# Performance work log

Hardware: AMD Instinct MI355X
Metric: run time of the kernel (lower is better)

The kernel has to match this reference:

```python
import jax, jax.numpy as jnp
import numpy as np

N_NODES = 100000


def _graph_conv(x, W, b, src, dst, n_nodes):
    # DGL GraphConv, norm='both':
    #   h = x * out_deg(src)^{-1/2}; h = h @ W; agg = scatter_sum over dst;
    #   out = agg * in_deg(dst)^{-1/2} + b
    ones = jnp.ones(src.shape, dtype=x.dtype)
    out_deg = jax.ops.segment_sum(ones, src, num_segments=n_nodes)
    in_deg = jax.ops.segment_sum(ones, dst, num_segments=n_nodes)
    norm_src = jax.lax.rsqrt(jnp.maximum(out_deg, 1.0))  # [N]
    norm_dst = jax.lax.rsqrt(jnp.maximum(in_deg, 1.0))   # [N]
    h = (x * norm_src[:, None]) @ W                      # [N, hid]
    msgs = h[src]                                        # [E, hid] gather
    agg = jax.ops.segment_sum(msgs, dst, num_segments=n_nodes)  # [N, hid]
    return jax.nn.relu(agg * norm_dst[:, None] + b)


def setup_inputs() -> dict:
    key = jax.random.key(0)
    k1, k2, k3, k4, k5 = jax.random.split(key, 5)
    n, e, d = N_NODES, 1600000, 128
    x = jax.random.normal(k1, (n, d), dtype=jnp.float32)
    src = jax.random.randint(k2, (e,), 0, n, dtype=jnp.int32)
    dst = jax.random.randint(k3, (e,), 0, n, dtype=jnp.int32)
    # Xavier-ish init for GraphConv weights, zero bias (DGL default)
    W1 = jax.random.normal(k4, (d, d), dtype=jnp.float32) / np.sqrt(d)
    W2 = jax.random.normal(k5, (d, d), dtype=jnp.float32) / np.sqrt(d)
    b1 = jnp.zeros((d,), dtype=jnp.float32)
    b2 = jnp.zeros((d,), dtype=jnp.float32)
    return {"x": x, "W1": W1, "b1": b1, "W2": W2, "b2": b2, "src": src, "dst": dst}


def reference(x, W1, b1, W2, b2, src, dst):
    h = _graph_conv(x, W1, b1, src, dst, N_NODES)
    h = _graph_conv(h, W2, b2, src, dst, N_NODES)
    return h
```

## Files before the change

### kernel.cpp

```cpp
#include <hip/hip_runtime.h>
#include <hip/hip_fp16.h>

#define HD 128
#define CHUNK 4096
#define MAXNB 512

__global__ __launch_bounds__(256) void count_src4(const int* __restrict__ src,
                                                  unsigned int* __restrict__ cnt4s,
                                                  int N, int E) {
    int t = blockIdx.x * 256 + threadIdx.x;
    int e0 = t * 4;
    if (e0 >= E) return;
    if (e0 + 3 < E) {
        int4 s4 = ((const int4*)src)[t];
        atomicAdd(&cnt4s[0 * N + s4.x], 1u);
        atomicAdd(&cnt4s[1 * N + s4.y], 1u);
        atomicAdd(&cnt4s[2 * N + s4.z], 1u);
        atomicAdd(&cnt4s[3 * N + s4.w], 1u);
    } else {
        for (int j = 0; e0 + j < E; ++j)
            atomicAdd(&cnt4s[j * N + src[e0 + j]], 1u);
    }
}

__global__ __launch_bounds__(256) void make_norm_src(const unsigned int* __restrict__ cnt4s,
                                                     float* __restrict__ norm_src, int N) {
    int i = blockIdx.x * 256 + threadIdx.x;
    if (i < N) {
        float od = (float)(cnt4s[i] + cnt4s[N + i] + cnt4s[2 * N + i] + cnt4s[3 * N + i]);
        norm_src[i] = rsqrtf(od > 1.f ? od : 1.f);
    }
}

__global__ __launch_bounds__(256) void hist_coarse(const int* __restrict__ dst,
                                                   unsigned int* __restrict__ gHist,
                                                   int NB, int NC, int E) {
    __shared__ unsigned int hist[MAXNB];
    for (int b = threadIdx.x; b < NB; b += 256) hist[b] = 0;
    __syncthreads();
    int chunk = blockIdx.x;
    int base = chunk * CHUNK;
    int end = base + CHUNK < E ? base + CHUNK : E;
    for (int e = base + threadIdx.x; e < end; e += 256)
        atomicAdd(&hist[dst[e] >> 8], 1u);
    __syncthreads();
    for (int b = threadIdx.x; b < NB; b += 256)
        gHist[(size_t)b * NC + chunk] = hist[b];
}

__global__ __launch_bounds__(256) void scan_a(const unsigned int* __restrict__ cnt,
                                              unsigned int* __restrict__ excl,
                                              unsigned int* __restrict__ bsum, int n) {
    int i = blockIdx.x * 256 + threadIdx.x;
    unsigned int v = (i < n) ? cnt[i] : 0u;
    unsigned int x = v;
#pragma unroll
    for (int d = 1; d < 64; d <<= 1) {
        unsigned int y = __shfl_up(x, d, 64);
        if ((threadIdx.x & 63) >= d) x += y;
    }
    __shared__ unsigned int wsum[4];
    if ((threadIdx.x & 63) == 63) wsum[threadIdx.x >> 6] = x;
    __syncthreads();
    unsigned int woff = 0;
    for (int w = 0; w < (int)(threadIdx.x >> 6); ++w) woff += wsum[w];
    unsigned int incl = x + woff;
    if (i < n) excl[i] = incl - v;
    if (threadIdx.x == 255) bsum[blockIdx.x] = incl;
}

__global__ __launch_bounds__(1024) void scan_b(const unsigned int* __restrict__ bsum,
                                               unsigned int* __restrict__ boff, int nb) {
    int t = threadIdx.x;
    unsigned int v = (t < nb) ? bsum[t] : 0u;
    unsigned int x = v;
#pragma unroll
    for (int d = 1; d < 64; d <<= 1) {
        unsigned int y = __shfl_up(x, d, 64);
        if ((t & 63) >= d) x += y;
    }
    __shared__ unsigned int wsum[16];
    if ((t & 63) == 63) wsum[t >> 6] = x;
    __syncthreads();
    unsigned int woff = 0;
    for (int w = 0; w < (t >> 6); ++w) woff += wsum[w];
    unsigned int incl = x + woff;
    if (t < nb) boff[t] = incl - v;
}

__global__ __launch_bounds__(256) void scan_c(unsigned int* __restrict__ excl,
                                              const unsigned int* __restrict__ boff, int n) {
    int i = blockIdx.x * 256 + threadIdx.x;
    if (i < n) excl[i] += boff[blockIdx.x];
}

__global__ __launch_bounds__(256) void scatter_coarse(const int* __restrict__ src,
                                                      const int* __restrict__ dst,
                                                      const unsigned int* __restrict__ scanA,
                                                      unsigned int* __restrict__ packed,
                                                      int NB, int NC, int E) {
    __shared__ unsigned int curs[MAXNB];
    int chunk = blockIdx.x;
    for (int b = threadIdx.x; b < NB; b += 256)
        curs[b] = scanA[(size_t)b * NC + chunk];
    __syncthreads();
    int base = chunk * CHUNK;
    int end = base + CHUNK < E ? base + CHUNK : E;
    for (int e = base + threadIdx.x; e < end; e += 256) {
        int d = dst[e];
        int s = src[e];
        unsigned int pos = atomicAdd(&curs[d >> 8], 1u);
        packed[pos] = ((unsigned int)(d & 255) << 24) | (unsigned int)s;
    }
}

__global__ __launch_bounds__(256) void fine_sort(const unsigned int* __restrict__ packed,
                                                 const unsigned int* __restrict__ scanA,
                                                 int* __restrict__ sorted_src,
                                                 unsigned int* __restrict__ offsets,
                                                 unsigned int* __restrict__ cntg,
                                                 float* __restrict__ normd,
                                                 int NB, int NC, int N, int E) {
    __shared__ unsigned int cnt[256];
    __shared__ unsigned int curs[256];
    __shared__ unsigned int wsum[4];
    int b = blockIdx.x;
    int t = threadIdx.x;
    unsigned int S = scanA[(size_t)b * NC];
    unsigned int T = (b + 1 < NB) ? scanA[(size_t)(b + 1) * NC] : (unsigned int)E;
    cnt[t] = 0;
    __syncthreads();
    for (unsigned int j = S + t; j < T; j += 256)
        atomicAdd(&cnt[packed[j] >> 24], 1u);
    __syncthreads();
    unsigned int v = cnt[t], x = v;
    int lane = t & 63;
#pragma unroll
    for (int d = 1; d < 64; d <<= 1) {
        unsigned int y = __shfl_up(x, d, 64);
        if (lane >= d) x += y;
    }
    if (lane == 63) wsum[t >> 6] = x;
    __syncthreads();
    unsigned int woff = 0;
    for (int w = 0; w < (t >> 6); ++w) woff += wsum[w];
    unsigned int ex = x - v + woff;
    curs[t] = ex;
    int node = b * 256 + t;
    if (node < N) {
        offsets[node] = S + ex;
        cntg[node] = v;
        float f = (float)v;
        normd[node] = rsqrtf(f > 1.f ? f : 1.f);
    }
    __syncthreads();
    for (unsigned int j = S + t; j < T; j += 256) {
        unsigned int p = packed[j];
        unsigned int pos = S + atomicAdd(&curs[p >> 24], 1u);
        sorted_src[pos] = (int)(p & 0xFFFFFFu);
    }
}

__global__ __launch_bounds__(256) void prep_x(const float* __restrict__ x,
                                              const float* __restrict__ norm,
                                              __half* __restrict__ xh, int total) {
    int t = blockIdx.x * 256 + threadIdx.x;
    if (t >= total) return;
    int row = t >> 5;
    float nr = norm[row];
    float4 v = ((const float4*)x)[t];
    __half2 lo = __floats2half2_rn(v.x * nr, v.y * nr);
    __half2 hi = __floats2half2_rn(v.z * nr, v.w * nr);
    uint2 pk;
    pk.x = *(unsigned int*)&lo;
    pk.y = *(unsigned int*)&hi;
    ((uint2*)xh)[t] = pk;
}

__global__ __launch_bounds__(256) void gemm_h(const __half* __restrict__ xh,
                                              const float* __restrict__ W,
                                              __half* __restrict__ h, int n) {
    __shared__ __half2 Wh[HD * 64];
    __shared__ float  xs[64][HD];
    const int tid = threadIdx.x;

    {
        const float4* W4 = (const float4*)W;
#pragma unroll
        for (int i = 0; i < 16; ++i) {
            int idx = tid + 256 * i;
            float4 wv = W4[idx];
            __half2 a = __floats2half2_rn(wv.x, wv.y);
            __half2 b = __floats2half2_rn(wv.z, wv.w);
            int k = idx >> 5, c4 = idx & 31;
            Wh[k * 64 + c4 * 2]     = a;
            Wh[k * 64 + c4 * 2 + 1] = b;
        }
    }
    const int row0 = blockIdx.x * 64;
    {
#pragma unroll
        for (int i = 0; i < 8; ++i) {
            int idx = i * 256 + tid;
            int r = idx >> 5, c = idx & 31;
            int row = row0 + r;
            uint2 u = make_uint2(0u, 0u);
            if (row < n) u = ((const uint2*)xh)[(size_t)row * 32 + c];
            float2 f0 = __half22float2(*(const __half2*)&u.x);
            float2 f1 = __half22float2(*(const __half2*)&u.y);
            ((float4*)xs[r])[c] = make_float4(f0.x, f0.y, f1.x, f1.y);
        }
    }
    __syncthreads();

    const int g  = tid >> 5;
    const int c4 = tid & 31;

    float4 acc[8];
#pragma unroll
    for (int j = 0; j < 8; ++j) acc[j] = make_float4(0.f, 0.f, 0.f, 0.f);

    for (int k = 0; k < HD; k += 2) {
        uint2 w0 = *(const uint2*)&Wh[k * 64 + c4 * 2];
        uint2 w1 = *(const uint2*)&Wh[(k + 1) * 64 + c4 * 2];
        float2 wa0 = __half22float2(*(const __half2*)&w0.x);
        float2 wb0 = __half22float2(*(const __half2*)&w0.y);
        float2 wa1 = __half22float2(*(const __half2*)&w1.x);
        float2 wb1 = __half22float2(*(const __half2*)&w1.y);
#pragma unroll
        for (int j = 0; j < 8; ++j) {
            float2 xk = *(const float2*)&xs[g * 8 + j][k];
            acc[j].x = fmaf(xk.x, wa0.x, acc[j].x);
            acc[j].y = fmaf(xk.x, wa0.y, acc[j].y);
            acc[j].z = fmaf(xk.x, wb0.x, acc[j].z);
            acc[j].w = fmaf(xk.x, wb0.y, acc[j].w);
            acc[j].x = fmaf(xk.y, wa1.x, acc[j].x);
            acc[j].y = fmaf(xk.y, wa1.y, acc[j].y);
            acc[j].z = fmaf(xk.y, wb1.x, acc[j].z);
            acc[j].w = fmaf(xk.y, wb1.y, acc[j].w);
        }
    }

#pragma unroll
    for (int j = 0; j < 8; ++j) {
        int row = row0 + g * 8 + j;
        if (row < n) {
            __half2 lo = __floats2half2_rn(acc[j].x, acc[j].y);
            __half2 hi = __floats2half2_rn(acc[j].z, acc[j].w);
            uint2 pk;
            pk.x = *(unsigned int*)&lo;
            pk.y = *(unsigned int*)&hi;
            ((uint2*)(h + (size_t)row * HD))[c4] = pk;
        }
    }
}

template <bool MID>
__global__ __launch_bounds__(256) void aggregate_k(const __half* __restrict__ h,
                                                   const int* __restrict__ sorted_src,
                                                   const unsigned int* __restrict__ offsets,
                                                   const unsigned int* __restrict__ cnt,
                                                   const float* __restrict__ norm_dst,
                                                   const float* __restrict__ nsrc,
                                                   const float* __restrict__ bias,
                                                   float* __restrict__ outF,
                                                   __half* __restrict__ outH, int n) {
    int node = blockIdx.x * 4 + (int)(threadIdx.x >> 6);
    if (node >= n) return;
    int lane = threadIdx.x & 63;
    int g   = lane >> 4;
    int sub = lane & 15;

    unsigned int start = offsets[node];
    unsigned int deg   = cnt[node];
    const int* sp = sorted_src + start;
    const uint4* h4 = (const uint4*)h;

    float acc[8];
#pragma unroll
    for (int j = 0; j < 8; ++j) acc[j] = 0.f;

#define ACCUM(u)                                                                  \
    { float2 f;                                                                   \
      f = __half22float2(*(const __half2*)&(u).x); acc[0] += f.x; acc[1] += f.y;  \
      f = __half22float2(*(const __half2*)&(u).y); acc[2] += f.x; acc[3] += f.y;  \
      f = __half22float2(*(const __half2*)&(u).z); acc[4] += f.x; acc[5] += f.y;  \
      f = __half22float2(*(const __half2*)&(u).w); acc[6] += f.x; acc[7] += f.y; }

    unsigned int i = 0;
    for (; i + 16 <= deg; i += 16) {
        int s0 = sp[i + g];
        int s1 = sp[i + 4 + g];
        int s2 = sp[i + 8 + g];
        int s3 = sp[i + 12 + g];
        uint4 u0 = h4[(size_t)s0 * 16 + sub];
        uint4 u1 = h4[(size_t)s1 * 16 + sub];
        uint4 u2 = h4[(size_t)s2 * 16 + sub];
        uint4 u3 = h4[(size_t)s3 * 16 + sub];
        ACCUM(u0);
        ACCUM(u1);
        ACCUM(u2);
        ACCUM(u3);
    }
    for (; i < deg; i += 4) {
        if (i + g < deg) {
            int s = sp[i + g];
            uint4 u = h4[(size_t)s * 16 + sub];
            ACCUM(u);
        }
    }
#undef ACCUM

#pragma unroll
    for (int j = 0; j < 8; ++j) {
        acc[j] += __shfl_xor(acc[j], 16, 64);
        acc[j] += __shfl_xor(acc[j], 32, 64);
    }

    float nd = norm_dst[node];
    int col2 = sub * 4 + g;
    float2 bb = ((const float2*)bias)[col2];
    float vx = fmaxf(fmaf(acc[g * 2 + 0], nd, bb.x), 0.f);
    float vy = fmaxf(fmaf(acc[g * 2 + 1], nd, bb.y), 0.f);
    if (MID) {
        float ns = nsrc[node];
        __half2 p = __floats2half2_rn(vx * ns, vy * ns);
        ((__half2*)outH)[(size_t)node * 64 + col2] = p;
    } else {
        ((float2*)outF)[(size_t)node * 64 + col2] = make_float2(vx, vy);
    }
}

extern "C" void kernel_launch(void* const* d_in, const int* in_sizes, int n_in,
                              void* d_out, int out_size, void* d_ws, size_t ws_size,
                              hipStream_t stream) {
    const float* x   = (const float*)d_in[0];
    const float* W1  = (const float*)d_in[1];
    const float* b1  = (const float*)d_in[2];
    const float* W2  = (const float*)d_in[3];
    const float* b2  = (const float*)d_in[4];
    const int*   src = (const int*)d_in[5];
    const int*   dst = (const int*)d_in[6];

    const int N = in_sizes[0] / HD;
    const int E = in_sizes[5];
    float* out = (float*)d_out;

    const int NB = (N + 255) / 256;
    const int NC = (E + CHUNK - 1) / CHUNK;
    const int scanLen = NB * NC;
    const int nbS = (scanLen + 255) / 256;
    const int nbN = (N + 255) / 256;

    float*        norm_src = (float*)d_ws;
    float*        normd    = norm_src + N;
    unsigned int* cntg     = (unsigned int*)(normd + N);
    unsigned int* offsets  = cntg + N;
    unsigned int* cnt4s    = offsets + N;
    unsigned int* gHist    = cnt4s + 4 * N;
    unsigned int* scanA    = gHist + scanLen;
    unsigned int* bsum     = scanA + scanLen;
    unsigned int* boff     = bsum + 1024;
    unsigned int* packed   = boff + 1024;
    int*          sorted   = (int*)(packed + E);
    __half*       h        = (__half*)(sorted + E);
    __half*       xh       = h + (size_t)N * HD;

    hipMemsetAsync(cnt4s, 0, (size_t)4 * N * 4, stream);
    count_src4<<<(E / 4 + 255) / 256, 256, 0, stream>>>(src, cnt4s, N, E);
    make_norm_src<<<nbN, 256, 0, stream>>>(cnt4s, norm_src, N);
    hist_coarse<<<NC, 256, 0, stream>>>(dst, gHist, NB, NC, E);
    scan_a<<<nbS, 256, 0, stream>>>(gHist, scanA, bsum, scanLen);
    scan_b<<<1, 1024, 0, stream>>>(bsum, boff, nbS);
    scan_c<<<nbS, 256, 0, stream>>>(scanA, boff, scanLen);
    scatter_coarse<<<NC, 256, 0, stream>>>(src, dst, scanA, packed, NB, NC, E);
    fine_sort<<<NB, 256, 0, stream>>>(packed, scanA, sorted, offsets, cntg, normd, NB, NC, N, E);

    prep_x<<<(N * 32 + 255) / 256, 256, 0, stream>>>(x, norm_src, xh, N * 32);
    gemm_h<<<(N + 63) / 64, 256, 0, stream>>>(xh, W1, h, N);
    aggregate_k<true><<<(N + 3) / 4, 256, 0, stream>>>(h, sorted, offsets, cntg, normd,
                                                       norm_src, b1, nullptr, xh, N);

    gemm_h<<<(N + 63) / 64, 256, 0, stream>>>(xh, W2, h, N);
    aggregate_k<false><<<(N + 3) / 4, 256, 0, stream>>>(h, sorted, offsets, cntg, normd,
                                                        nullptr, b2, out, nullptr, N);
}
```

Measured before the change: 398.3 us.

## Use MFMA fp16 GEMM with pre-transposed weights and fuse degree histograms

Replaces the scalar-FMA LDS-tiled GEMM with a register-only MFMA 16x16x32 f16 kernel. It reads x rows and pre-transposed fp16 weights, which a new prep_w kernel builds once for both layers. The src out-degree count and the coarse dst histogram now run in one kernel, so there is one fewer launch and the edge arrays are read in a single pass. Buffers are padded to a multiple of 64 rows so the GEMM can read rows past N without bounds checks. The risk is that weight fragments now come from global/L2 memory and are not shared in LDS.

```diff
diff --git a/kernel.cpp b/kernel.cpp
--- a/kernel.cpp
+++ b/kernel.cpp
@@ -5,22 +5,43 @@
 #define CHUNK 4096
 #define MAXNB 512
 
-__global__ __launch_bounds__(256) void count_src4(const int* __restrict__ src,
+typedef _Float16 f16x8 __attribute__((ext_vector_type(8)));
+typedef float f32x4 __attribute__((ext_vector_type(4)));
+
+__global__ __launch_bounds__(256) void hist_count(const int* __restrict__ src,
+                                                  const int* __restrict__ dst,
                                                   unsigned int* __restrict__ cnt4s,
-                                                  int N, int E) {
-    int t = blockIdx.x * 256 + threadIdx.x;
-    int e0 = t * 4;
-    if (e0 >= E) return;
-    if (e0 + 3 < E) {
-        int4 s4 = ((const int4*)src)[t];
-        atomicAdd(&cnt4s[0 * N + s4.x], 1u);
-        atomicAdd(&cnt4s[1 * N + s4.y], 1u);
-        atomicAdd(&cnt4s[2 * N + s4.z], 1u);
-        atomicAdd(&cnt4s[3 * N + s4.w], 1u);
-    } else {
-        for (int j = 0; e0 + j < E; ++j)
-            atomicAdd(&cnt4s[j * N + src[e0 + j]], 1u);
-    }
+                                                  unsigned int* __restrict__ gHist,
+                                                  int N, int NB, int NC, int E) {
+    __shared__ unsigned int hist[MAXNB];
+    for (int b = threadIdx.x; b < NB; b += 256) hist[b] = 0;
+    __syncthreads();
+    int base = blockIdx.x * CHUNK;
+    int e0 = base + 4 * threadIdx.x;
+#pragma unroll
+    for (int it = 0; it < CHUNK / 1024; ++it, e0 += 1024) {
+        if (e0 + 3 < E) {
+            int4 s4 = *(const int4*)(src + e0);
+            int4 d4 = *(const int4*)(dst + e0);
+            atomicAdd(&cnt4s[0 * N + s4.x], 1u);
+            atomicAdd(&cnt4s[1 * N + s4.y], 1u);
+            atomicAdd(&cnt4s[2 * N + s4.z], 1u);
+            atomicAdd(&cnt4s[3 * N + s4.w], 1u);
+            atomicAdd(&hist[d4.x >> 8], 1u);
+            atomicAdd(&hist[d4.y >> 8], 1u);
+            atomicAdd(&hist[d4.z >> 8], 1u);
+            atomicAdd(&hist[d4.w >> 8], 1u);
+        } else {
+            for (int j = 0; j < 4; ++j)
+                if (e0 + j < E) {
+                    atomicAdd(&cnt4s[j * N + src[e0 + j]], 1u);
+                    atomicAdd(&hist[dst[e0 + j] >> 8], 1u);
+                }
+        }
+    }
+    __syncthreads();
+    for (int b = threadIdx.x; b < NB; b += 256)
+        gHist[(size_t)b * NC + blockIdx.x] = hist[b];
 }
 
 __global__ __launch_bounds__(256) void make_norm_src(const unsigned int* __restrict__ cnt4s,
@@ -32,20 +53,15 @@
     }
 }
 
-__global__ __launch_bounds__(256) void hist_coarse(const int* __restrict__ dst,
-                                                   unsigned int* __restrict__ gHist,
-                                                   int NB, int NC, int E) {
-    __shared__ unsigned int hist[MAXNB];
-    for (int b = threadIdx.x; b < NB; b += 256) hist[b] = 0;
-    __syncthreads();
-    int chunk = blockIdx.x;
-    int base = chunk * CHUNK;
-    int end = base + CHUNK < E ? base + CHUNK : E;
-    for (int e = base + threadIdx.x; e < end; e += 256)
-        atomicAdd(&hist[dst[e] >> 8], 1u);
-    __syncthreads();
-    for (int b = threadIdx.x; b < NB; b += 256)
-        gHist[(size_t)b * NC + chunk] = hist[b];
+__global__ __launch_bounds__(256) void prep_w(const float* __restrict__ W1,
+                                              const float* __restrict__ W2,
+                                              _Float16* __restrict__ Wt) {
+    const float* W = blockIdx.x ? W2 : W1;
+    _Float16* T = Wt + (size_t)blockIdx.x * HD * HD;
+    for (int i = threadIdx.x; i < HD * HD; i += 256) {
+        int k = i >> 7, c = i & 127;
+        T[c * HD + k] = (_Float16)W[i];
+    }
 }
 
 __global__ __launch_bounds__(256) void scan_a(const unsigned int* __restrict__ cnt,
@@ -163,7 +179,7 @@
 
 __global__ __launch_bounds__(256) void prep_x(const float* __restrict__ x,
                                               const float* __restrict__ norm,
-                                              __half* __restrict__ xh, int total) {
+                                              _Float16* __restrict__ xh, int total) {
     int t = blockIdx.x * 256 + threadIdx.x;
     if (t >= total) return;
     int row = t >> 5;
@@ -177,80 +193,46 @@
     ((uint2*)xh)[t] = pk;
 }
 
-__global__ __launch_bounds__(256) void gemm_h(const __half* __restrict__ xh,
-                                              const float* __restrict__ W,
-                                              __half* __restrict__ h, int n) {
-    __shared__ __half2 Wh[HD * 64];
-    __shared__ float  xs[64][HD];
+__global__ __launch_bounds__(256) void gemm_mfma(const _Float16* __restrict__ xh,
+                                                 const _Float16* __restrict__ Wt,
+                                                 _Float16* __restrict__ h, int n) {
     const int tid = threadIdx.x;
-
-    {
-        const float4* W4 = (const float4*)W;
-#pragma unroll
-        for (int i = 0; i < 16; ++i) {
-            int idx = tid + 256 * i;
-            float4 wv = W4[idx];
-            __half2 a = __floats2half2_rn(wv.x, wv.y);
-            __half2 b = __floats2half2_rn(wv.z, wv.w);
-            int k = idx >> 5, c4 = idx & 31;
-            Wh[k * 64 + c4 * 2]     = a;
-            Wh[k * 64 + c4 * 2 + 1] = b;
+    const int w  = tid >> 6;
+    const int l  = tid & 63;
+    const int lg = l >> 4;
+    const int li = l & 15;
+    const int m  = blockIdx.x * 64 + w * 16 + li;
+
+    const _Float16* xrow = xh + (size_t)m * HD + lg * 8;
+    f16x8 xf[4];
+#pragma unroll
+    for (int kk = 0; kk < 4; ++kk)
+        xf[kk] = *(const f16x8*)(xrow + kk * 32);
+
+    f32x4 acc[8];
+#pragma unroll
+    for (int t = 0; t < 8; ++t) acc[t] = (f32x4){0.f, 0.f, 0.f, 0.f};
+
+#pragma unroll
+    for (int t = 0; t < 8; ++t) {
+        const _Float16* wrow = Wt + (size_t)(t * 16 + li) * HD + lg * 8;
+#pragma unroll
+        for (int kk = 0; kk < 4; ++kk) {
+            f16x8 wf = *(const f16x8*)(wrow + kk * 32);
+            acc[t] = __builtin_amdgcn_mfma_f32_16x16x32_f16(wf, xf[kk], acc[t], 0, 0, 0);
         }
     }
-    const int row0 = blockIdx.x * 64;
-    {
-#pragma unroll
-        for (int i = 0; i < 8; ++i) {
-            int idx = i * 256 + tid;
-            int r = idx >> 5, c = idx & 31;
-            int row = row0 + r;
-            uint2 u = make_uint2(0u, 0u);
-            if (row < n) u = ((const uint2*)xh)[(size_t)row * 32 + c];
-            float2 f0 = __half22float2(*(const __half2*)&u.x);
-            float2 f1 = __half22float2(*(const __half2*)&u.y);
-            ((float4*)xs[r])[c] = make_float4(f0.x, f0.y, f1.x, f1.y);
-        }
-    }
-    __syncthreads();
-
-    const int g  = tid >> 5;
-    const int c4 = tid & 31;
-
-    float4 acc[8];
-#pragma unroll
-    for (int j = 0; j < 8; ++j) acc[j] = make_float4(0.f, 0.f, 0.f, 0.f);
-
-    for (int k = 0; k < HD; k += 2) {
-        uint2 w0 = *(const uint2*)&Wh[k * 64 + c4 * 2];
-        uint2 w1 = *(const uint2*)&Wh[(k + 1) * 64 + c4 * 2];
-        float2 wa0 = __half22float2(*(const __half2*)&w0.x);
-        float2 wb0 = __half22float2(*(const __half2*)&w0.y);
-        float2 wa1 = __half22float2(*(const __half2*)&w1.x);
-        float2 wb1 = __half22float2(*(const __half2*)&w1.y);
-#pragma unroll
-        for (int j = 0; j < 8; ++j) {
-            float2 xk = *(const float2*)&xs[g * 8 + j][k];
-            acc[j].x = fmaf(xk.x, wa0.x, acc[j].x);
-            acc[j].y = fmaf(xk.x, wa0.y, acc[j].y);
-            acc[j].z = fmaf(xk.x, wb0.x, acc[j].z);
-            acc[j].w = fmaf(xk.x, wb0.y, acc[j].w);
-            acc[j].x = fmaf(xk.y, wa1.x, acc[j].x);
-            acc[j].y = fmaf(xk.y, wa1.y, acc[j].y);
-            acc[j].z = fmaf(xk.y, wb1.x, acc[j].z);
-            acc[j].w = fmaf(xk.y, wb1.y, acc[j].w);
-        }
-    }
-
-#pragma unroll
-    for (int j = 0; j < 8; ++j) {
-        int row = row0 + g * 8 + j;
-        if (row < n) {
-            __half2 lo = __floats2half2_rn(acc[j].x, acc[j].y);
-            __half2 hi = __floats2half2_rn(acc[j].z, acc[j].w);
+
+    if (m < n) {
+        _Float16* hp = h + (size_t)m * HD + lg * 4;
+#pragma unroll
+        for (int t = 0; t < 8; ++t) {
+            __half2 p0 = __floats2half2_rn(acc[t][0], acc[t][1]);
+            __half2 p1 = __floats2half2_rn(acc[t][2], acc[t][3]);
             uint2 pk;
-            pk.x = *(unsigned int*)&lo;
-            pk.y = *(unsigned int*)&hi;
-            ((uint2*)(h + (size_t)row * HD))[c4] = pk;
+            pk.x = *(unsigned int*)&p0;
+            pk.y = *(unsigned int*)&p1;
+            *(uint2*)(hp + t * 16) = pk;
         }
     }
 }
@@ -346,6 +328,7 @@
     const int E = in_sizes[5];
     float* out = (float*)d_out;
 
+    const int NP = (N + 63) & ~63;
     const int NB = (N + 255) / 256;
     const int NC = (E + CHUNK - 1) / CHUNK;
     const int scanLen = NB * NC;
@@ -363,13 +346,14 @@
     unsigned int* boff     = bsum + 1024;
     unsigned int* packed   = boff + 1024;
     int*          sorted   = (int*)(packed + E);
-    __half*       h        = (__half*)(sorted + E);
-    __half*       xh       = h + (size_t)N * HD;
+    _Float16*     h        = (_Float16*)(sorted + E);
+    _Float16*     xh       = h + (size_t)NP * HD;
+    _Float16*     Wt       = xh + (size_t)NP * HD;
 
     hipMemsetAsync(cnt4s, 0, (size_t)4 * N * 4, stream);
-    count_src4<<<(E / 4 + 255) / 256, 256, 0, stream>>>(src, cnt4s, N, E);
+    prep_w<<<2, 256, 0, stream>>>(W1, W2, Wt);
+    hist_count<<<NC, 256, 0, stream>>>(src, dst, cnt4s, gHist, N, NB, NC, E);
     make_norm_src<<<nbN, 256, 0, stream>>>(cnt4s, norm_src, N);
-    hist_coarse<<<NC, 256, 0, stream>>>(dst, gHist, NB, NC, E);
     scan_a<<<nbS, 256, 0, stream>>>(gHist, scanA, bsum, scanLen);
     scan_b<<<1, 1024, 0, stream>>>(bsum, boff, nbS);
     scan_c<<<nbS, 256, 0, stream>>>(scanA, boff, scanLen);
@@ -377,11 +361,12 @@
     fine_sort<<<NB, 256, 0, stream>>>(packed, scanA, sorted, offsets, cntg, normd, NB, NC, N, E);
 
     prep_x<<<(N * 32 + 255) / 256, 256, 0, stream>>>(x, norm_src, xh, N * 32);
-    gemm_h<<<(N + 63) / 64, 256, 0, stream>>>(xh, W1, h, N);
-    aggregate_k<true><<<(N + 3) / 4, 256, 0, stream>>>(h, sorted, offsets, cntg, normd,
-                                                       norm_src, b1, nullptr, xh, N);
-
-    gemm_h<<<(N + 63) / 64, 256, 0, stream>>>(xh, W2, h, N);
-    aggregate_k<false><<<(N + 3) / 4, 256, 0, stream>>>(h, sorted, offsets, cntg, normd,
-                                                        nullptr, b2, out, nullptr, N);
-}
+    gemm_mfma<<<NP / 64, 256, 0, stream>>>(xh, Wt, h, N);
+    aggregate_k<true><<<(N + 3) / 4, 256, 0, stream>>>((const __half*)h, sorted, offsets, cntg,
+                                                       normd, norm_src, b1, nullptr,
+                                                       (__half*)xh, N);
+
+    gemm_mfma<<<NP / 64, 256, 0, stream>>>(xh, Wt + HD * HD, h, N);
+    aggregate_k<false><<<(N + 3) / 4, 256, 0, stream>>>((const __half*)h, sorted, offsets, cntg,
+                                                        normd, nullptr, b2, out, nullptr, N);
+}
```

Result: faster. 369.7 us (-7.2%).
